# Optimization experiments

Measured on AMD Instinct MI355X. Metric: run time of the kernel, lower is better.

The kernel has to match this reference:

```python
import jax, jax.numpy as jnp
import numpy as np
import math

EMBED = 1024
HEADS = 16
HEAD_DIM = EMBED // HEADS
B, S = 2, 2048


def setup_inputs() -> dict:
    key = jax.random.key(0)
    ks = jax.random.split(key, 12)
    sc = 1.0 / math.sqrt(EMBED)
    inp = {
        'query': jax.random.normal(ks[0], (B, S, EMBED), jnp.float32),
        'key': jax.random.normal(ks[1], (B, S, EMBED), jnp.float32),
        'values': jax.random.normal(ks[2], (B, S, EMBED), jnp.float32),
        # causal mask, broadcastable to [B, H, S, S]; masked where == 0
        'mask': jnp.tril(jnp.ones((S, S), jnp.int32))[None, None, :, :],
        'Wq': jax.random.normal(ks[3], (EMBED, EMBED), jnp.float32) * sc,
        'bq': jnp.zeros((EMBED,), jnp.float32),
        'Wk': jax.random.normal(ks[4], (EMBED, EMBED), jnp.float32) * sc,
        'bk': jnp.zeros((EMBED,), jnp.float32),
        'Wv': jax.random.normal(ks[5], (EMBED, EMBED), jnp.float32) * sc,
        'bv': jnp.zeros((EMBED,), jnp.float32),
        'Wo': jax.random.normal(ks[6], (EMBED, EMBED), jnp.float32) * sc,
        'bo': jnp.zeros((EMBED,), jnp.float32),
    }
    return inp


def reference(query, key, values, mask, Wq, bq, Wk, bk, Wv, bv, Wo, bo):
    # linear projections (torch Linear: x @ W.T + b)
    q = query @ Wq.T + bq
    k = key @ Wk.T + bk
    v = values @ Wv.T + bv
    b, sq, _ = q.shape
    sk = k.shape[1]
    q = q.reshape(b, sq, HEADS, HEAD_DIM)  # bqhd
    k = k.reshape(b, sk, HEADS, HEAD_DIM)  # bkhd
    v = v.reshape(b, sk, HEADS, HEAD_DIM)  # bkhd
    energy = jnp.einsum('bqhd,bkhd->bhqk', q, k) / math.sqrt(HEAD_DIM)
    energy = jnp.where(mask == 0, jnp.float32(-1e10), energy)
    attn = jax.nn.softmax(energy, axis=-1)
    out = jnp.einsum('bhqk,bkhd->bqhd', attn, v).reshape(b, sq, EMBED)
    return out @ Wo.T + bo
```

## Files before the change

### kernel.cpp

```cpp
#include <hip/hip_runtime.h>

typedef unsigned short u16;
typedef unsigned int   u32;
typedef __attribute__((ext_vector_type(4)))  float f32x4;
typedef __attribute__((ext_vector_type(8)))  short bf16x8;
typedef __attribute__((ext_vector_type(4)))  u32   u32x4;
typedef __attribute__((ext_vector_type(4)))  u16   u16x4;

#define AS1 __attribute__((address_space(1)))
#define AS3 __attribute__((address_space(3)))

__device__ __forceinline__ u16 f2bf(float f) {
  union { float f; u32 u; } v; v.f = f;
  u32 r = v.u + 0x7FFFu + ((v.u >> 16) & 1u);
  return (u16)(r >> 16);
}

__device__ __forceinline__ u16 f2bf_t(float f) {
  union { float f; u32 u; } v; v.f = f;
  return (u16)(v.u >> 16);
}

__device__ __forceinline__ void g2l16(const void* g, void* l) {
  __builtin_amdgcn_global_load_lds((const AS1 u32*)g, (AS3 u32*)l, 16, 0, 0);
}

struct CvtArgs {
  const float* src[7];
  u16*         dst[7];
  int          n4[7];
};

__global__ __launch_bounds__(256) void cvt_kernel(CvtArgs a) {
  const int ai = blockIdx.y;
  const f32x4* s = (const f32x4*)a.src[ai];
  u16x4*       d = (u16x4*)a.dst[ai];
  const int n4 = a.n4[ai];
  for (int i = blockIdx.x * 256 + threadIdx.x; i < n4; i += gridDim.x * 256) {
    f32x4 v = s[i];
    u16x4 o;
    o[0] = f2bf(v[0]); o[1] = f2bf(v[1]); o[2] = f2bf(v[2]); o[3] = f2bf(v[3]);
    d[i] = o;
  }
}

template <typename OutT, int TM>
__device__ __forceinline__ void gemm_core64(
    const u16* __restrict__ A, const u16* __restrict__ W,
    const float* __restrict__ bias, bool rowbias,
    OutT* __restrict__ C, int ldc, int row0, int col0,
    u16* sA, u16* sB, int tid)
{
  constexpr int K = 1024;
  constexpr int MF = TM / 32;
  const int lane = tid & 63, wid = tid >> 6;
  const int l15 = lane & 15, hi = lane >> 4;
  const int wr = (wid >> 1) * (TM / 2), wc = (wid & 1) * 64;

  f32x4 acc[MF][4];
#pragma unroll
  for (int i = 0; i < MF; ++i)
#pragma unroll
    for (int j = 0; j < 4; ++j) acc[i][j] = f32x4{0.f, 0.f, 0.f, 0.f};

  auto stage = [&](int kt) {
#pragma unroll
    for (int it = 0; it < TM / 32; ++it) {
      int idx = it * 256 + tid;
      int r = idx >> 3, g = idx & 7;
      int gs = g ^ (r & 7);
      g2l16(A + (size_t)(row0 + r) * K + kt * 64 + gs * 8, sA + idx * 8);
    }
#pragma unroll
    for (int it = 0; it < 4; ++it) {
      int idx = it * 256 + tid;
      int r = idx >> 3, g = idx & 7;
      int gs = g ^ (r & 7);
      g2l16(W + (size_t)(col0 + r) * K + kt * 64 + gs * 8, sB + idx * 8);
    }
  };

  stage(0);
  for (int kt = 0; kt < K / 64; ++kt) {
    __syncthreads();
    bf16x8 aF[MF][2], bF[4][2];
#pragma unroll
    for (int mf = 0; mf < MF; ++mf) {
      int r = wr + mf * 16 + l15;
#pragma unroll
      for (int kh = 0; kh < 2; ++kh)
        aF[mf][kh] = *(const bf16x8*)(sA + r * 64 + ((kh * 4 + hi) ^ (r & 7)) * 8);
    }
#pragma unroll
    for (int nf = 0; nf < 4; ++nf) {
      int r = wc + nf * 16 + l15;
#pragma unroll
      for (int kh = 0; kh < 2; ++kh)
        bF[nf][kh] = *(const bf16x8*)(sB + r * 64 + ((kh * 4 + hi) ^ (r & 7)) * 8);
    }
    __syncthreads();
    if (kt + 1 < K / 64) stage(kt + 1);
#pragma unroll
    for (int kh = 0; kh < 2; ++kh)
#pragma unroll
      for (int mf = 0; mf < MF; ++mf)
#pragma unroll
        for (int nf = 0; nf < 4; ++nf)
          acc[mf][nf] = __builtin_amdgcn_mfma_f32_16x16x32_bf16(aF[mf][kh], bF[nf][kh], acc[mf][nf], 0, 0, 0);
  }

#pragma unroll
  for (int nf = 0; nf < 4; ++nf) {
    int gcol = col0 + wc + nf * 16 + l15;
    float bcol = rowbias ? 0.f : bias[gcol];
#pragma unroll
    for (int mf = 0; mf < MF; ++mf) {
#pragma unroll
      for (int r = 0; r < 4; ++r) {
        int grow = row0 + wr + mf * 16 + hi * 4 + r;
        float bv = rowbias ? bias[grow] : bcol;
        float v = acc[mf][nf][r] + bv;
        if constexpr (sizeof(OutT) == 2) {
          ((u16*)C)[(size_t)grow * ldc + gcol] = f2bf(v);
        } else {
          ((float*)C)[(size_t)grow * ldc + gcol] = v;
        }
      }
    }
  }
}

struct ProjArgs {
  const u16* A[3]; const u16* W[3]; const float* bias[3];
  u16* C[3];
};

__global__ __launch_bounds__(256, 2) void gemm_proj(ProjArgs p) {
  __shared__ alignas(16) u16 sA[128 * 64];
  __shared__ alignas(16) u16 sB[128 * 64];
  const int w = (blockIdx.x & 7) * 96 + (blockIdx.x >> 3);
  int which, row0, col0, ldc;
  bool rowbias;
  if (w < 512) {
    which = w >> 8;
    int l = w & 255;
    col0 = (l & 7) << 7;
    row0 = (l >> 3) << 7;
    ldc = 1024; rowbias = false;
  } else {
    which = 2;
    int l = w - 512;
    col0 = (l & 31) << 7;
    row0 = (l >> 5) << 7;
    ldc = 4096; rowbias = true;
  }
  gemm_core64<u16, 128>(p.A[which], p.W[which], p.bias[which], rowbias,
                        p.C[which], ldc, row0, col0, sA, sB, threadIdx.x);
}

__global__ __launch_bounds__(256, 2) void gemm_out(
    const u16* __restrict__ A, const u16* __restrict__ W,
    const float* __restrict__ bias, float* __restrict__ C)
{
  __shared__ alignas(16) u16 sA[64 * 64];
  __shared__ alignas(16) u16 sB[128 * 64];
  const int w = (blockIdx.x & 7) * 64 + (blockIdx.x >> 3);
  const int col0 = (w & 7) << 7;
  const int row0 = (w >> 3) << 6;
  gemm_core64<float, 64>(A, W, bias, false, C, 1024, row0, col0, sA, sB, threadIdx.x);
}

__global__ __launch_bounds__(256, 4) void attn_fwd(
    const u16* __restrict__ Q, const u16* __restrict__ Kg, const u16* __restrict__ VT,
    u16* __restrict__ ctx)
{
  __shared__ alignas(16) u16 sK[2][64 * 64];
  __shared__ alignas(16) u16 sVt[2][64 * 64];
  __shared__ alignas(16) u16 sP[4][16 * 64];

  const int tid = threadIdx.x;
  const int lane = tid & 63, wid = tid >> 6;
  const int l15 = lane & 15, hi = lane >> 4;

  const int wg = blockIdx.x;
  const int jj = wg >> 5, bh = wg & 31;
  const int rr = jj >> 3, kk = jj & 7;
  int xt;
  if (rr == 0)      xt = 31 - kk;
  else if (rr == 1) xt = 16 + kk;
  else if (rr == 2) xt = 15 - kk;
  else              xt = kk;

  const int b = bh >> 4, h = bh & 15;
  const int q0 = xt * 64;
  const int q0w = q0 + wid * 16;
  const size_t base  = ((size_t)b * 2048) * 1024 + h * 64;
  const size_t vbase = (size_t)(h * 64) * 4096 + b * 2048;

  bf16x8 qf[2];
#pragma unroll
  for (int kh = 0; kh < 2; ++kh)
    qf[kh] = *(const bf16x8*)(Q + base + (size_t)(q0w + l15) * 1024 + kh * 32 + hi * 8);

  f32x4 o[4];
  float lS[4];
#pragma unroll
  for (int nf = 0; nf < 4; ++nf) o[nf] = f32x4{0.f, 0.f, 0.f, 0.f};
#pragma unroll
  for (int r = 0; r < 4; ++r) lS[r] = 0.f;

  u16* sPw = &sP[wid][0];
  const int nt = xt + 1;

  auto issueK = [&](int ti, int bb) {
#pragma unroll
    for (int it = 0; it < 2; ++it) {
      int idx = it * 256 + tid;
      int r = idx >> 3, g = idx & 7;
      int gs = g ^ (r & 7);
      g2l16(Kg + base + (size_t)(ti * 64 + r) * 1024 + gs * 8, &sK[bb][idx * 8]);
    }
  };
  auto issueV = [&](int ti, int bb) {
#pragma unroll
    for (int it = 0; it < 2; ++it) {
      int idx = it * 256 + tid;
      int r = idx >> 3, g = idx & 7;
      int gs = g ^ (r & 7);
      g2l16(VT + vbase + (size_t)r * 4096 + ti * 64 + gs * 8, &sVt[bb][idx * 8]);
    }
  };

  issueK(0, 0);
  issueV(0, 0);
  __syncthreads();

  constexpr float SCL = 0.125f * 1.44269504f;

  for (int ti = 0; ti < nt; ++ti) {
    const int cur = ti & 1;
    const bool pf = (ti + 1 < nt);
    if (pf) {
      issueK(ti + 1, cur ^ 1);
      issueV(ti + 1, cur ^ 1);
    }

    const int kv0 = ti * 64;
    const bool needmask = (ti == xt);
    const u16* sKc = &sK[cur][0];
    const u16* sVc = &sVt[cur][0];

    f32x4 s[4];
#pragma unroll
    for (int n = 0; n < 4; ++n) s[n] = f32x4{0.f, 0.f, 0.f, 0.f};
#pragma unroll
    for (int n = 0; n < 4; ++n) {
      int kvr = n * 16 + l15;
      bf16x8 kf0 = *(const bf16x8*)(sKc + kvr * 64 + ((hi) ^ (kvr & 7)) * 8);
      bf16x8 kf1 = *(const bf16x8*)(sKc + kvr * 64 + ((4 + hi) ^ (kvr & 7)) * 8);
      s[n] = __builtin_amdgcn_mfma_f32_16x16x32_bf16(qf[0], kf0, s[n], 0, 0, 0);
      s[n] = __builtin_amdgcn_mfma_f32_16x16x32_bf16(qf[1], kf1, s[n], 0, 0, 0);
    }

#pragma unroll
    for (int r = 0; r < 4; ++r) {
      float lsum = 0.f;
#pragma unroll
      for (int n = 0; n < 4; ++n) {
        float sv = s[n][r] * SCL;
        if (needmask) {
          int qa = q0w + hi * 4 + r;
          int ka = kv0 + n * 16 + l15;
          if (ka > qa) sv = -1e30f;
        }
        float p = __builtin_amdgcn_exp2f(sv);
        s[n][r] = p;
        lsum += p;
      }
      lS[r] += lsum;
    }

#pragma unroll
    for (int n = 0; n < 4; ++n) {
      int c = n * 16 + l15;
#pragma unroll
      for (int r = 0; r < 4; ++r) {
        int q = hi * 4 + r;
        sPw[q * 64 + (c ^ ((q & 7) << 3))] = f2bf_t(s[n][r]);
      }
    }

#pragma unroll
    for (int kq = 0; kq < 2; ++kq) {
      bf16x8 pa, vb[4];
      pa = *(const bf16x8*)(sPw + l15 * 64 + ((kq * 32 + hi * 8) ^ ((l15 & 7) << 3)));
#pragma unroll
      for (int nf = 0; nf < 4; ++nf) {
        int rd = nf * 16 + l15;
        vb[nf] = *(const bf16x8*)(sVc + rd * 64 + ((kq * 4 + hi) ^ (rd & 7)) * 8);
      }
#pragma unroll
      for (int nf = 0; nf < 4; ++nf)
        o[nf] = __builtin_amdgcn_mfma_f32_16x16x32_bf16(pa, vb[nf], o[nf], 0, 0, 0);
    }

    __syncthreads();
  }

#pragma unroll
  for (int r = 0; r < 4; ++r) {
    float t = lS[r];
    t += __shfl_xor(t, 1);
    t += __shfl_xor(t, 2);
    t += __shfl_xor(t, 4);
    t += __shfl_xor(t, 8);
    float inv = 1.f / t;
    size_t rowoff = base + (size_t)(q0w + hi * 4 + r) * 1024;
#pragma unroll
    for (int nf = 0; nf < 4; ++nf)
      ctx[rowoff + nf * 16 + l15] = f2bf(o[nf][r] * inv);
  }
}

extern "C" void kernel_launch(void* const* d_in, const int* in_sizes, int n_in,
                              void* d_out, int out_size, void* d_ws, size_t ws_size,
                              hipStream_t stream) {
  const float* query = (const float*)d_in[0];
  const float* key   = (const float*)d_in[1];
  const float* vals  = (const float*)d_in[2];
  const float* Wq = (const float*)d_in[4];
  const float* bq = (const float*)d_in[5];
  const float* Wk = (const float*)d_in[6];
  const float* bk = (const float*)d_in[7];
  const float* Wv = (const float*)d_in[8];
  const float* bv = (const float*)d_in[9];
  const float* Wo = (const float*)d_in[10];
  const float* bo = (const float*)d_in[11];
  float* out = (float*)d_out;

  if (ws_size < 58720256) return;

  u16* ws = (u16*)d_ws;
  u16* xq = ws + 0;
  u16* xk = ws + 4194304;
  u16* xv = ws + 8388608;
  u16* wq = ws + 12582912;
  u16* wk = ws + 13631488;
  u16* wv = ws + 14680064;
  u16* wo = ws + 15728640;
  u16* Qb = ws + 16777216;
  u16* Kb = ws + 20971520;
  u16* VT = ws + 25165824;
  u16* ctx = xq;

  CvtArgs ca;
  ca.src[0] = query; ca.dst[0] = xq; ca.n4[0] = 1048576;
  ca.src[1] = key;   ca.dst[1] = xk; ca.n4[1] = 1048576;
  ca.src[2] = vals;  ca.dst[2] = xv; ca.n4[2] = 1048576;
  ca.src[3] = Wq;    ca.dst[3] = wq; ca.n4[3] = 262144;
  ca.src[4] = Wk;    ca.dst[4] = wk; ca.n4[4] = 262144;
  ca.src[5] = Wv;    ca.dst[5] = wv; ca.n4[5] = 262144;
  ca.src[6] = Wo;    ca.dst[6] = wo; ca.n4[6] = 262144;
  cvt_kernel<<<dim3(256, 7), 256, 0, stream>>>(ca);

  ProjArgs pa;
  pa.A[0] = xq; pa.W[0] = wq; pa.bias[0] = bq; pa.C[0] = Qb;
  pa.A[1] = xk; pa.W[1] = wk; pa.bias[1] = bk; pa.C[1] = Kb;
  pa.A[2] = wv; pa.W[2] = xv; pa.bias[2] = bv; pa.C[2] = VT;
  gemm_proj<<<dim3(768), 256, 0, stream>>>(pa);

  attn_fwd<<<dim3(1024), 256, 0, stream>>>(Qb, Kb, VT, ctx);

  gemm_out<<<dim3(512), 256, 0, stream>>>(ctx, wo, bo, out);
}
```

Before: 106.8 us.

## Pair complementary causal query tiles per attention block to share K/V loads

Each attention workgroup now handles two query tiles, xt and 31-xt, so every block does the same number of KV steps and each K/V tile loaded into LDS serves both query tiles. The grid halves to 512 blocks and launch bounds drop from 4 to 2 waves per SIMD to leave room for the doubled accumulators. This aims to cut K/V global and LDS traffic and remove load imbalance from the causal mask. The cost is fewer resident waves for latency hiding and a serial dependency on the shared per-wave sP buffer between the two phases.

```diff
diff --git a/kernel.cpp b/kernel.cpp
--- a/kernel.cpp
+++ b/kernel.cpp
@@ -170,7 +170,7 @@
   gemm_core64<float, 64>(A, W, bias, false, C, 1024, row0, col0, sA, sB, threadIdx.x);
 }
 
-__global__ __launch_bounds__(256, 4) void attn_fwd(
+__global__ __launch_bounds__(256, 2) void attn_fwd(
     const u16* __restrict__ Q, const u16* __restrict__ Kg, const u16* __restrict__ VT,
     u16* __restrict__ ctx)
 {
@@ -182,35 +182,32 @@
   const int lane = tid & 63, wid = tid >> 6;
   const int l15 = lane & 15, hi = lane >> 4;
 
-  const int wg = blockIdx.x;
-  const int jj = wg >> 5, bh = wg & 31;
-  const int rr = jj >> 3, kk = jj & 7;
-  int xt;
-  if (rr == 0)      xt = 31 - kk;
-  else if (rr == 1) xt = 16 + kk;
-  else if (rr == 2) xt = 15 - kk;
-  else              xt = kk;
-
+  const int bid = blockIdx.x;
+  const int jj = bid >> 5, bh = bid & 31;
+  const int pr = (jj < 8) ? jj : 23 - jj;
+  const int xtA = pr, xtB = 31 - pr;
+  const int steps = xtB + 1;
   const int b = bh >> 4, h = bh & 15;
-  const int q0 = xt * 64;
-  const int q0w = q0 + wid * 16;
+  const int q0A = xtA * 64 + wid * 16;
+  const int q0B = xtB * 64 + wid * 16;
   const size_t base  = ((size_t)b * 2048) * 1024 + h * 64;
   const size_t vbase = (size_t)(h * 64) * 4096 + b * 2048;
 
-  bf16x8 qf[2];
-#pragma unroll
-  for (int kh = 0; kh < 2; ++kh)
-    qf[kh] = *(const bf16x8*)(Q + base + (size_t)(q0w + l15) * 1024 + kh * 32 + hi * 8);
-
-  f32x4 o[4];
-  float lS[4];
-#pragma unroll
-  for (int nf = 0; nf < 4; ++nf) o[nf] = f32x4{0.f, 0.f, 0.f, 0.f};
-#pragma unroll
-  for (int r = 0; r < 4; ++r) lS[r] = 0.f;
+  bf16x8 qfA[2], qfB[2];
+#pragma unroll
+  for (int kh = 0; kh < 2; ++kh) {
+    qfA[kh] = *(const bf16x8*)(Q + base + (size_t)(q0A + l15) * 1024 + kh * 32 + hi * 8);
+    qfB[kh] = *(const bf16x8*)(Q + base + (size_t)(q0B + l15) * 1024 + kh * 32 + hi * 8);
+  }
+
+  f32x4 oA[4], oB[4];
+  float lA[4], lB[4];
+#pragma unroll
+  for (int nf = 0; nf < 4; ++nf) { oA[nf] = f32x4{0.f, 0.f, 0.f, 0.f}; oB[nf] = f32x4{0.f, 0.f, 0.f, 0.f}; }
+#pragma unroll
+  for (int r = 0; r < 4; ++r) { lA[r] = 0.f; lB[r] = 0.f; }
 
   u16* sPw = &sP[wid][0];
-  const int nt = xt + 1;
 
   auto issueK = [&](int ti, int bb) {
 #pragma unroll
@@ -237,31 +234,8 @@
 
   constexpr float SCL = 0.125f * 1.44269504f;
 
-  for (int ti = 0; ti < nt; ++ti) {
-    const int cur = ti & 1;
-    const bool pf = (ti + 1 < nt);
-    if (pf) {
-      issueK(ti + 1, cur ^ 1);
-      issueV(ti + 1, cur ^ 1);
-    }
-
-    const int kv0 = ti * 64;
-    const bool needmask = (ti == xt);
-    const u16* sKc = &sK[cur][0];
-    const u16* sVc = &sVt[cur][0];
-
-    f32x4 s[4];
-#pragma unroll
-    for (int n = 0; n < 4; ++n) s[n] = f32x4{0.f, 0.f, 0.f, 0.f};
-#pragma unroll
-    for (int n = 0; n < 4; ++n) {
-      int kvr = n * 16 + l15;
-      bf16x8 kf0 = *(const bf16x8*)(sKc + kvr * 64 + ((hi) ^ (kvr & 7)) * 8);
-      bf16x8 kf1 = *(const bf16x8*)(sKc + kvr * 64 + ((4 + hi) ^ (kvr & 7)) * 8);
-      s[n] = __builtin_amdgcn_mfma_f32_16x16x32_bf16(qf[0], kf0, s[n], 0, 0, 0);
-      s[n] = __builtin_amdgcn_mfma_f32_16x16x32_bf16(qf[1], kf1, s[n], 0, 0, 0);
-    }
-
+  auto phase = [&](f32x4 (&s)[4], bool needmask, int q0w, int kv0,
+                   const u16* sVc, f32x4 (&o)[4], float (&lS)[4]) {
 #pragma unroll
     for (int r = 0; r < 4; ++r) {
       float lsum = 0.f;
@@ -279,7 +253,6 @@
       }
       lS[r] += lsum;
     }
-
 #pragma unroll
     for (int n = 0; n < 4; ++n) {
       int c = n * 16 + l15;
@@ -289,7 +262,6 @@
         sPw[q * 64 + (c ^ ((q & 7) << 3))] = f2bf_t(s[n][r]);
       }
     }
-
 #pragma unroll
     for (int kq = 0; kq < 2; ++kq) {
       bf16x8 pa, vb[4];
@@ -303,22 +275,66 @@
       for (int nf = 0; nf < 4; ++nf)
         o[nf] = __builtin_amdgcn_mfma_f32_16x16x32_bf16(pa, vb[nf], o[nf], 0, 0, 0);
     }
+  };
+
+  for (int ti = 0; ti < steps; ++ti) {
+    const int cur = ti & 1;
+    const bool pf = (ti + 1 < steps);
+    if (pf) {
+      issueK(ti + 1, cur ^ 1);
+      issueV(ti + 1, cur ^ 1);
+    }
+
+    const int kv0 = ti * 64;
+    const bool doA = (ti <= xtA);
+    const u16* sKc = &sK[cur][0];
+    const u16* sVc = &sVt[cur][0];
+
+    f32x4 sa[4], sb[4];
+#pragma unroll
+    for (int n = 0; n < 4; ++n) { sa[n] = f32x4{0.f, 0.f, 0.f, 0.f}; sb[n] = f32x4{0.f, 0.f, 0.f, 0.f}; }
+#pragma unroll
+    for (int n = 0; n < 4; ++n) {
+      int kvr = n * 16 + l15;
+      bf16x8 kf0 = *(const bf16x8*)(sKc + kvr * 64 + ((hi) ^ (kvr & 7)) * 8);
+      bf16x8 kf1 = *(const bf16x8*)(sKc + kvr * 64 + ((4 + hi) ^ (kvr & 7)) * 8);
+      sb[n] = __builtin_amdgcn_mfma_f32_16x16x32_bf16(qfB[0], kf0, sb[n], 0, 0, 0);
+      sb[n] = __builtin_amdgcn_mfma_f32_16x16x32_bf16(qfB[1], kf1, sb[n], 0, 0, 0);
+      if (doA) {
+        sa[n] = __builtin_amdgcn_mfma_f32_16x16x32_bf16(qfA[0], kf0, sa[n], 0, 0, 0);
+        sa[n] = __builtin_amdgcn_mfma_f32_16x16x32_bf16(qfA[1], kf1, sa[n], 0, 0, 0);
+      }
+    }
+
+    phase(sb, ti == xtB, q0B, kv0, sVc, oB, lB);
+    if (doA) phase(sa, ti == xtA, q0A, kv0, sVc, oA, lA);
 
     __syncthreads();
   }
 
 #pragma unroll
   for (int r = 0; r < 4; ++r) {
-    float t = lS[r];
-    t += __shfl_xor(t, 1);
-    t += __shfl_xor(t, 2);
-    t += __shfl_xor(t, 4);
-    t += __shfl_xor(t, 8);
-    float inv = 1.f / t;
-    size_t rowoff = base + (size_t)(q0w + hi * 4 + r) * 1024;
+    float tB = lB[r];
+    tB += __shfl_xor(tB, 1);
+    tB += __shfl_xor(tB, 2);
+    tB += __shfl_xor(tB, 4);
+    tB += __shfl_xor(tB, 8);
+    float invB = 1.f / tB;
+    size_t rowB = base + (size_t)(q0B + hi * 4 + r) * 1024;
 #pragma unroll
     for (int nf = 0; nf < 4; ++nf)
-      ctx[rowoff + nf * 16 + l15] = f2bf(o[nf][r] * inv);
+      ctx[rowB + nf * 16 + l15] = f2bf(oB[nf][r] * invB);
+
+    float tA = lA[r];
+    tA += __shfl_xor(tA, 1);
+    tA += __shfl_xor(tA, 2);
+    tA += __shfl_xor(tA, 4);
+    tA += __shfl_xor(tA, 8);
+    float invA = 1.f / tA;
+    size_t rowA = base + (size_t)(q0A + hi * 4 + r) * 1024;
+#pragma unroll
+    for (int nf = 0; nf < 4; ++nf)
+      ctx[rowA + nf * 16 + l15] = f2bf(oA[nf][r] * invA);
   }
 }
 
@@ -369,7 +385,7 @@
   pa.A[2] = wv; pa.W[2] = xv; pa.bias[2] = bv; pa.C[2] = VT;
   gemm_proj<<<dim3(768), 256, 0, stream>>>(pa);
 
-  attn_fwd<<<dim3(1024), 256, 0, stream>>>(Qb, Kb, VT, ctx);
+  attn_fwd<<<dim3(512), 256, 0, stream>>>(Qb, Kb, VT, ctx);
 
   gemm_out<<<dim3(512), 256, 0, stream>>>(ctx, wo, bo, out);
 }
```

Result: no change. 108.2 us (+1.3%).

## Fuse fp32-to-bf16 activation conversion into projection GEMM staging

Applied to the files above, without the earlier changes.

The separate conversion pass for query/key/values is removed. The projection GEMM now loads fp32 activations directly, rounds them to bf16 in registers and stores them into the swizzled shared tiles, while weights are still pre-converted. This avoids writing and re-reading the bf16 activation copies, at the cost of synchronous global loads in place of async global-to-LDS copies, and of each activation tile being reconverted by every column block.

```diff
diff --git a/kernel.cpp b/kernel.cpp
--- a/kernel.cpp
+++ b/kernel.cpp
@@ -6,6 +6,7 @@
 typedef __attribute__((ext_vector_type(8)))  short bf16x8;
 typedef __attribute__((ext_vector_type(4)))  u32   u32x4;
 typedef __attribute__((ext_vector_type(4)))  u16   u16x4;
+typedef __attribute__((ext_vector_type(8)))  u16   u16x8;
 
 #define AS1 __attribute__((address_space(1)))
 #define AS3 __attribute__((address_space(3)))
@@ -21,14 +22,19 @@
   return (u16)(v.u >> 16);
 }
 
+__device__ __forceinline__ u16 rbf(float f) {
+  union { float f; u32 u; } v; v.f = f;
+  return (u16)((v.u + 0x8000u) >> 16);
+}
+
 __device__ __forceinline__ void g2l16(const void* g, void* l) {
   __builtin_amdgcn_global_load_lds((const AS1 u32*)g, (AS3 u32*)l, 16, 0, 0);
 }
 
 struct CvtArgs {
-  const float* src[7];
-  u16*         dst[7];
-  int          n4[7];
+  const float* src[4];
+  u16*         dst[4];
+  int          n4[4];
 };
 
 __global__ __launch_bounds__(256) void cvt_kernel(CvtArgs a) {
@@ -46,7 +52,8 @@
 
 template <typename OutT, int TM>
 __device__ __forceinline__ void gemm_core64(
-    const u16* __restrict__ A, const u16* __restrict__ W,
+    const void* __restrict__ Aop, bool af32,
+    const void* __restrict__ Wop, bool wf32,
     const float* __restrict__ bias, bool rowbias,
     OutT* __restrict__ C, int ldc, int row0, int col0,
     u16* sA, u16* sB, int tid)
@@ -63,21 +70,32 @@
 #pragma unroll
     for (int j = 0; j < 4; ++j) acc[i][j] = f32x4{0.f, 0.f, 0.f, 0.f};
 
+  auto stageOp = [&](const void* P, bool f32src, u16* dst, int r0, int kt, int iters) {
+    if (!f32src) {
+      for (int it = 0; it < iters; ++it) {
+        int idx = it * 256 + tid;
+        int r = idx >> 3, g = idx & 7;
+        int gs = g ^ (r & 7);
+        g2l16((const u16*)P + (size_t)(r0 + r) * K + kt * 64 + gs * 8, dst + idx * 8);
+      }
+    } else {
+      for (int it = 0; it < iters; ++it) {
+        int idx = it * 256 + tid;
+        int r = idx >> 3, g = idx & 7;
+        int gs = g ^ (r & 7);
+        const float* s = (const float*)P + (size_t)(r0 + r) * K + kt * 64 + gs * 8;
+        f32x4 v0 = *(const f32x4*)s;
+        f32x4 v1 = *(const f32x4*)(s + 4);
+        u16x8 w;
+        w[0] = rbf(v0[0]); w[1] = rbf(v0[1]); w[2] = rbf(v0[2]); w[3] = rbf(v0[3]);
+        w[4] = rbf(v1[0]); w[5] = rbf(v1[1]); w[6] = rbf(v1[2]); w[7] = rbf(v1[3]);
+        *(u16x8*)(dst + idx * 8) = w;
+      }
+    }
+  };
   auto stage = [&](int kt) {
-#pragma unroll
-    for (int it = 0; it < TM / 32; ++it) {
-      int idx = it * 256 + tid;
-      int r = idx >> 3, g = idx & 7;
-      int gs = g ^ (r & 7);
-      g2l16(A + (size_t)(row0 + r) * K + kt * 64 + gs * 8, sA + idx * 8);
-    }
-#pragma unroll
-    for (int it = 0; it < 4; ++it) {
-      int idx = it * 256 + tid;
-      int r = idx >> 3, g = idx & 7;
-      int gs = g ^ (r & 7);
-      g2l16(W + (size_t)(col0 + r) * K + kt * 64 + gs * 8, sB + idx * 8);
-    }
+    stageOp(Aop, af32, sA, row0, kt, TM / 32);
+    stageOp(Wop, wf32, sB, col0, kt, 4);
   };
 
   stage(0);
@@ -131,8 +149,9 @@
 }
 
 struct ProjArgs {
-  const u16* A[3]; const u16* W[3]; const float* bias[3];
+  const void* A[3]; const void* W[3]; const float* bias[3];
   u16* C[3];
+  int af32[3], wf32[3];
 };
 
 __global__ __launch_bounds__(256, 2) void gemm_proj(ProjArgs p) {
@@ -154,7 +173,9 @@
     row0 = (l >> 5) << 7;
     ldc = 4096; rowbias = true;
   }
-  gemm_core64<u16, 128>(p.A[which], p.W[which], p.bias[which], rowbias,
+  gemm_core64<u16, 128>(p.A[which], p.af32[which] != 0,
+                        p.W[which], p.wf32[which] != 0,
+                        p.bias[which], rowbias,
                         p.C[which], ldc, row0, col0, sA, sB, threadIdx.x);
 }
 
@@ -167,7 +188,8 @@
   const int w = (blockIdx.x & 7) * 64 + (blockIdx.x >> 3);
   const int col0 = (w & 7) << 7;
   const int row0 = (w >> 3) << 6;
-  gemm_core64<float, 64>(A, W, bias, false, C, 1024, row0, col0, sA, sB, threadIdx.x);
+  gemm_core64<float, 64>(A, false, W, false, bias, false, C, 1024, row0, col0,
+                         sA, sB, threadIdx.x);
 }
 
 __global__ __launch_bounds__(256, 4) void attn_fwd(
@@ -338,35 +360,29 @@
   const float* bo = (const float*)d_in[11];
   float* out = (float*)d_out;
 
-  if (ws_size < 58720256) return;
+  if (ws_size < 41943040) return;
 
   u16* ws = (u16*)d_ws;
-  u16* xq = ws + 0;
-  u16* xk = ws + 4194304;
-  u16* xv = ws + 8388608;
-  u16* wq = ws + 12582912;
-  u16* wk = ws + 13631488;
-  u16* wv = ws + 14680064;
-  u16* wo = ws + 15728640;
-  u16* Qb = ws + 16777216;
-  u16* Kb = ws + 20971520;
-  u16* VT = ws + 25165824;
-  u16* ctx = xq;
+  u16* wq = ws + 0;
+  u16* wk = ws + 1048576;
+  u16* wv = ws + 2097152;
+  u16* wo = ws + 3145728;
+  u16* Qb = ws + 4194304;
+  u16* Kb = ws + 8388608;
+  u16* VT = ws + 12582912;
+  u16* ctx = ws + 16777216;
 
   CvtArgs ca;
-  ca.src[0] = query; ca.dst[0] = xq; ca.n4[0] = 1048576;
-  ca.src[1] = key;   ca.dst[1] = xk; ca.n4[1] = 1048576;
-  ca.src[2] = vals;  ca.dst[2] = xv; ca.n4[2] = 1048576;
-  ca.src[3] = Wq;    ca.dst[3] = wq; ca.n4[3] = 262144;
-  ca.src[4] = Wk;    ca.dst[4] = wk; ca.n4[4] = 262144;
-  ca.src[5] = Wv;    ca.dst[5] = wv; ca.n4[5] = 262144;
-  ca.src[6] = Wo;    ca.dst[6] = wo; ca.n4[6] = 262144;
-  cvt_kernel<<<dim3(256, 7), 256, 0, stream>>>(ca);
+  ca.src[0] = Wq; ca.dst[0] = wq; ca.n4[0] = 262144;
+  ca.src[1] = Wk; ca.dst[1] = wk; ca.n4[1] = 262144;
+  ca.src[2] = Wv; ca.dst[2] = wv; ca.n4[2] = 262144;
+  ca.src[3] = Wo; ca.dst[3] = wo; ca.n4[3] = 262144;
+  cvt_kernel<<<dim3(128, 4), 256, 0, stream>>>(ca);
 
   ProjArgs pa;
-  pa.A[0] = xq; pa.W[0] = wq; pa.bias[0] = bq; pa.C[0] = Qb;
-  pa.A[1] = xk; pa.W[1] = wk; pa.bias[1] = bk; pa.C[1] = Kb;
-  pa.A[2] = wv; pa.W[2] = xv; pa.bias[2] = bv; pa.C[2] = VT;
+  pa.A[0] = query; pa.W[0] = wq;   pa.bias[0] = bq; pa.C[0] = Qb; pa.af32[0] = 1; pa.wf32[0] = 0;
+  pa.A[1] = key;   pa.W[1] = wk;   pa.bias[1] = bk; pa.C[1] = Kb; pa.af32[1] = 1; pa.wf32[1] = 0;
+  pa.A[2] = wv;    pa.W[2] = vals; pa.bias[2] = bv; pa.C[2] = VT; pa.af32[2] = 0; pa.wf32[2] = 1;
   gemm_proj<<<dim3(768), 256, 0, stream>>>(pa);
 
   attn_fwd<<<dim3(1024), 256, 0, stream>>>(Qb, Kb, VT, ctx);
```

Result: slower. 130.5 us (+22.2%).

## Split long causal query tiles across two KV-range workgroups and merge partials

Applied to the files above, without the earlier changes.

The attention kernel now gives each of the 16 longest causal query tiles per head two workgroups: one covers KV tiles 0–15 and the other covers 16 up to the diagonal. Shorter tiles still run in a single pass and write the context directly. Split tiles write unnormalized fp32 partial outputs and row sums into workspace, and a new merge kernel adds them and normalizes to bf16. The goal is to shorten the critical path set by the longest workgroups. In exchange it adds an extra kernel launch plus the fp32 partial write and read traffic.

```diff
diff --git a/kernel.cpp b/kernel.cpp
--- a/kernel.cpp
+++ b/kernel.cpp
@@ -172,7 +172,7 @@
 
 __global__ __launch_bounds__(256, 4) void attn_fwd(
     const u16* __restrict__ Q, const u16* __restrict__ Kg, const u16* __restrict__ VT,
-    u16* __restrict__ ctx)
+    u16* __restrict__ ctx, float* __restrict__ Opart, float* __restrict__ Lpart)
 {
   __shared__ alignas(16) u16 sK[2][64 * 64];
   __shared__ alignas(16) u16 sVt[2][64 * 64];
@@ -182,18 +182,20 @@
   const int lane = tid & 63, wid = tid >> 6;
   const int l15 = lane & 15, hi = lane >> 4;
 
-  const int wg = blockIdx.x;
-  const int jj = wg >> 5, bh = wg & 31;
-  const int rr = jj >> 3, kk = jj & 7;
-  int xt;
-  if (rr == 0)      xt = 31 - kk;
-  else if (rr == 1) xt = 16 + kk;
-  else if (rr == 2) xt = 15 - kk;
-  else              xt = kk;
+  const int bh = blockIdx.x & 31;
+  const int j  = blockIdx.x >> 5;
+  int xt, ts, te, slot;
+  bool direct;
+  if (j < 16) {
+    xt = 16 + j; ts = 0; te = 15; slot = 0; direct = false;
+  } else {
+    int m = j - 16;
+    if ((m & 1) == 0) { xt = 31 - (m >> 1); ts = 16; te = xt; slot = 1; direct = false; }
+    else              { xt = 15 - (m >> 1); ts = 0;  te = xt; slot = 0; direct = true;  }
+  }
 
   const int b = bh >> 4, h = bh & 15;
-  const int q0 = xt * 64;
-  const int q0w = q0 + wid * 16;
+  const int q0w = xt * 64 + wid * 16;
   const size_t base  = ((size_t)b * 2048) * 1024 + h * 64;
   const size_t vbase = (size_t)(h * 64) * 4096 + b * 2048;
 
@@ -210,7 +212,6 @@
   for (int r = 0; r < 4; ++r) lS[r] = 0.f;
 
   u16* sPw = &sP[wid][0];
-  const int nt = xt + 1;
 
   auto issueK = [&](int ti, int bb) {
 #pragma unroll
@@ -231,15 +232,15 @@
     }
   };
 
-  issueK(0, 0);
-  issueV(0, 0);
+  issueK(ts, 0);
+  issueV(ts, 0);
   __syncthreads();
 
   constexpr float SCL = 0.125f * 1.44269504f;
 
-  for (int ti = 0; ti < nt; ++ti) {
-    const int cur = ti & 1;
-    const bool pf = (ti + 1 < nt);
+  for (int ti = ts; ti <= te; ++ti) {
+    const int cur = (ti - ts) & 1;
+    const bool pf = (ti < te);
     if (pf) {
       issueK(ti + 1, cur ^ 1);
       issueV(ti + 1, cur ^ 1);
@@ -314,11 +315,47 @@
     t += __shfl_xor(t, 2);
     t += __shfl_xor(t, 4);
     t += __shfl_xor(t, 8);
-    float inv = 1.f / t;
-    size_t rowoff = base + (size_t)(q0w + hi * 4 + r) * 1024;
-#pragma unroll
-    for (int nf = 0; nf < 4; ++nf)
-      ctx[rowoff + nf * 16 + l15] = f2bf(o[nf][r] * inv);
+    if (direct) {
+      float inv = 1.f / t;
+      size_t rowoff = base + (size_t)(q0w + hi * 4 + r) * 1024;
+#pragma unroll
+      for (int nf = 0; nf < 4; ++nf)
+        ctx[rowoff + nf * 16 + l15] = f2bf(o[nf][r] * inv);
+    } else {
+      int qr = wid * 16 + hi * 4 + r;
+      size_t pidx = ((size_t)(bh * 16 + (xt - 16)) * 2 + slot);
+      float* Op = Opart + (pidx * 64 + qr) * 64;
+#pragma unroll
+      for (int nf = 0; nf < 4; ++nf)
+        Op[nf * 16 + l15] = o[nf][r];
+      if (l15 == 0) Lpart[pidx * 64 + qr] = t;
+    }
+  }
+}
+
+__global__ __launch_bounds__(256) void attn_merge(
+    const float* __restrict__ Opart, const float* __restrict__ Lpart,
+    u16* __restrict__ ctx)
+{
+  const int bid = blockIdx.x;
+  const int bh = bid >> 4, px = bid & 15;
+  const int b = bh >> 4, h = bh & 15;
+  const int xt = 16 + px;
+  const size_t pidx = ((size_t)(bh * 16 + px) * 2);
+  const float* O0 = Opart + (pidx + 0) * 4096;
+  const float* O1 = Opart + (pidx + 1) * 4096;
+  const float* L0 = Lpart + (pidx + 0) * 64;
+  const float* L1 = Lpart + (pidx + 1) * 64;
+  const size_t base = ((size_t)b * 2048) * 1024 + h * 64;
+
+  const int tid = threadIdx.x;
+#pragma unroll
+  for (int e = 0; e < 16; ++e) {
+    int idx = e * 256 + tid;
+    int q = idx >> 6, d = idx & 63;
+    float l = L0[q] + L1[q];
+    float ov = O0[idx] + O1[idx];
+    ctx[base + (size_t)(xt * 64 + q) * 1024 + d] = f2bf(ov / l);
   }
 }
 
@@ -352,6 +389,8 @@
   u16* Kb = ws + 20971520;
   u16* VT = ws + 25165824;
   u16* ctx = xq;
+  float* Opart = (float*)(ws + 4194304);
+  float* Lpart = (float*)(ws + 12582912);
 
   CvtArgs ca;
   ca.src[0] = query; ca.dst[0] = xq; ca.n4[0] = 1048576;
@@ -369,7 +408,8 @@
   pa.A[2] = wv; pa.W[2] = xv; pa.bias[2] = bv; pa.C[2] = VT;
   gemm_proj<<<dim3(768), 256, 0, stream>>>(pa);
 
-  attn_fwd<<<dim3(1024), 256, 0, stream>>>(Qb, Kb, VT, ctx);
+  attn_fwd<<<dim3(1536), 256, 0, stream>>>(Qb, Kb, VT, ctx, Opart, Lpart);
+  attn_merge<<<dim3(512), 256, 0, stream>>>(Opart, Lpart, ctx);
 
   gemm_out<<<dim3(512), 256, 0, stream>>>(ctx, wo, bo, out);
 }
```

After: 111.2 us. 4.2% more time.
